# Kernel optimization log

Hardware: AMD Instinct MI355X
Metric: run time of the kernel (lower is better)

Reference implementation:

```python
import jax, jax.numpy as jnp
import numpy as np

B, K, E, D = 256, 2, 16, 512  # batch, top_k, num_experts, input_dim==output_dim
EPS = 1e-5  # nn.LayerNorm default eps
SCALE = 0.02  # param init scale


def setup_inputs() -> dict:
    key = jax.random.key(0)
    ks = jax.random.split(key, 9)
    return {
        "x": jax.random.normal(ks[0], (B, D), dtype=jnp.float32),
        "weight_probs": jax.random.uniform(ks[1], (B, K), dtype=jnp.float32),
        "bias_probs": jax.random.uniform(ks[2], (B, K), dtype=jnp.float32),
        "input_weight_bank": jax.random.normal(ks[3], (E, D, D), dtype=jnp.float32) * SCALE,
        "output_weight_bank": jax.random.normal(ks[4], (E, D, D), dtype=jnp.float32) * SCALE,
        "diagonal_weight_bank": jax.random.normal(ks[5], (E, D, D), dtype=jnp.float32) * SCALE,
        "bias_bank": jax.random.normal(ks[6], (E, D, D), dtype=jnp.float32) * SCALE,
        "weight_indices": jax.random.randint(ks[7], (B, K), 0, E),
        "bias_indices": jax.random.randint(ks[8], (B, K), 0, E),
    }


def reference(x, weight_probs, bias_probs, input_weight_bank, output_weight_bank,
              diagonal_weight_bank, bias_bank, weight_indices, bias_indices):
    # gather per-example expert parameter slabs: [B, K, D, D]
    iv = jnp.einsum('bi,bkij->bkj', x, input_weight_bank[weight_indices])     # [B,K,D]
    ov = jnp.einsum('bi,bkij->bkj', x, output_weight_bank[weight_indices])    # [B,K,D]
    dv = jnp.einsum('bi,bkij->bkj', x, diagonal_weight_bank[weight_indices])  # [B,K,D]

    # outer-product generated weight matrix + dynamic diagonal (in==out, no padding)
    outer = iv[..., :, None] * ov[..., None, :]                               # [B,K,D,D]
    r = jnp.arange(D)
    W = outer.at[..., r, r].add(dv)                                           # add diag embed

    # probability-weighted combine over top-k (weight_probs reshaped (-1,K,1,1) in torch)
    Wmix = jnp.einsum('bk,bkio->bio', weight_probs, W)                        # [B,D,D]

    # LayerNorm over output_dim, elementwise_affine=False
    mu = jnp.mean(Wmix, axis=-1, keepdims=True)
    var = jnp.var(Wmix, axis=-1, keepdims=True)
    Wn = (Wmix - mu) * jax.lax.rsqrt(var + EPS)

    # generated biases: gather + einsum + weighted combine ((-1,K,1) reshape)
    bv = jnp.einsum('bi,bkio->bko', x, bias_bank[bias_indices])               # [B,K,D]
    bmix = jnp.einsum('bk,bko->bo', bias_probs, bv)                           # [B,D]
    return (Wn, bmix)
```

## Files before the change

kernel.cpp:

```cpp
#include <hip/hip_runtime.h>
#include <math.h>

#define BB 256
#define KK 2
#define EE 16
#define DD 512
#define BK (BB*KK)
#define NP 4

#define WCH 18432
#define BCH 18560
#define WS_F_BASE 20480
#define SLAB (BK*DD)

__global__ void build_lists(const int* __restrict__ widx,
                            const int* __restrict__ bidx,
                            int* __restrict__ ws) {
    __shared__ int scw[16], scb[16];
    int* wlist = ws + 1024;
    int* blist = ws + 10240;
    const int t = threadIdx.x;
    if (t < 16) { scw[t] = 0; scb[t] = 0; }
    __syncthreads();
    int e = widx[t];
    int p = atomicAdd(&scw[e], 1);
    wlist[e * BK + p] = t;
    int eb = bidx[t];
    int pb = atomicAdd(&scb[eb], 1);
    blist[eb * BK + pb] = t;
    __syncthreads();
    if (t == 0) {
        int nc = 0;
        for (int e2 = 0; e2 < 16; ++e2) {
            int n = scw[e2];
            for (int r = 0; r < n; r += 16)
                ws[WCH + 1 + nc++] = e2 | (r << 8) | (min(16, n - r) << 20);
        }
        ws[WCH] = nc;
    }
    if (t == 64) {
        int nc = 0;
        for (int e2 = 0; e2 < 16; ++e2) {
            int n = scb[e2];
            for (int r = 0; r < n; r += 16)
                ws[BCH + 1 + nc++] = e2 | (r << 8) | (min(16, n - r) << 20);
        }
        ws[BCH] = nc;
    }
}

__launch_bounds__(256)
__global__ void expert_vm(const float* __restrict__ x,
                          const float* __restrict__ w_in,
                          const float* __restrict__ w_out,
                          const float* __restrict__ w_diag,
                          const float* __restrict__ w_bias,
                          const int* __restrict__ ws_i,
                          float* __restrict__ ws_f) {
    const int zp = blockIdx.z;
    const int z = zp >> 2, ip = zp & 3;
    const int* ch = ws_i + ((z < 3) ? WCH : BCH);
    const int slot = blockIdx.y;
    if (slot >= ch[0]) return;
    const int desc = ch[1 + slot];
    const int e = desc & 0xff, r0 = (desc >> 8) & 0xfff, rows = desc >> 20;
    const int* list = ws_i + ((z < 3) ? 1024 : 10240) + e * BK + r0;
    const int i0 = ip * 128;
    const float* W = (z == 0 ? w_in : z == 1 ? w_out : z == 2 ? w_diag : w_bias)
                     + (size_t)e * DD * DD + (size_t)i0 * DD;
    float* out = ws_f + WS_F_BASE + (size_t)zp * SLAB;

    __shared__ int plist[16];
    __shared__ float4 xs[128][4];
    const int t = threadIdx.x;
    if (t < 16) plist[t] = (t < rows) ? list[t] : -1;
    __syncthreads();
    #pragma unroll
    for (int k = 0; k < 2; ++k) {
        int idx = t + k * 256;
        int i = idx >> 2, q = idx & 3;
        int p0 = plist[q * 4 + 0], p1 = plist[q * 4 + 1];
        int p2 = plist[q * 4 + 2], p3 = plist[q * 4 + 3];
        float4 v;
        v.x = (p0 >= 0) ? x[(p0 >> 1) * DD + i0 + i] : 0.f;
        v.y = (p1 >= 0) ? x[(p1 >> 1) * DD + i0 + i] : 0.f;
        v.z = (p2 >= 0) ? x[(p2 >> 1) * DD + i0 + i] : 0.f;
        v.w = (p3 >= 0) ? x[(p3 >> 1) * DD + i0 + i] : 0.f;
        xs[i][q] = v;
    }
    __syncthreads();

    const int col = blockIdx.x * 128 + (t & 127);
    const int h = t >> 7;
    const float* Wc = W + col;
    float a0 = 0, a1 = 0, a2 = 0, a3 = 0, b0 = 0, b1 = 0, b2 = 0, b3 = 0;
    #pragma unroll 16
    for (int i = 0; i < 128; ++i) {
        float w = Wc[(size_t)i * DD];
        float4 xa = xs[i][2 * h];
        float4 xb = xs[i][2 * h + 1];
        a0 += xa.x * w; a1 += xa.y * w; a2 += xa.z * w; a3 += xa.w * w;
        b0 += xb.x * w; b1 += xb.y * w; b2 += xb.z * w; b3 += xb.w * w;
    }
    float accs[8] = {a0, a1, a2, a3, b0, b1, b2, b3};
    #pragma unroll
    for (int r = 0; r < 8; ++r) {
        int p = plist[h * 8 + r];
        if (p >= 0) out[(size_t)p * DD + col] = accs[r];
    }
}

__launch_bounds__(256)
__global__ void gen_write(const float* __restrict__ ws_f,
                          const float* __restrict__ wp,
                          float* __restrict__ outp) {
    const int b = blockIdx.y;
    const int chunk = blockIdx.x;
    const float* base = ws_f + WS_F_BASE;

    __shared__ float4 ov1v[128], ov2v[128];
    __shared__ float S[5], red[20];
    __shared__ float sa1[64], sa2[64], sdd[64], smu[64], srs[64];
    const int t = threadIdx.x;
    const float* ov1 = (const float*)ov1v;
    const float* ov2 = (const float*)ov2v;

    {
        const int tt = t & 127;
        const int row = b * 2 + (t >> 7);
        float sx = 0.f, sy = 0.f, sz = 0.f, sw = 0.f;
        #pragma unroll
        for (int pp = 0; pp < NP; ++pp) {
            const float4* q4 = (const float4*)(base + (size_t)(4 + pp) * SLAB
                                               + (size_t)row * DD);
            float4 v = q4[tt];
            sx += v.x; sy += v.y; sz += v.z; sw += v.w;
        }
        float4 s = make_float4(sx, sy, sz, sw);
        if (t < 128) ov1v[tt] = s; else ov2v[tt] = s;
    }
    __syncthreads();

    float v0a = ov1[t], v0b = ov1[t + 256], v1a = ov2[t], v1b = ov2[t + 256];
    float s[5];
    s[0] = v0a + v0b;
    s[1] = v1a + v1b;
    s[2] = v0a * v0a + v0b * v0b;
    s[3] = v0a * v1a + v0b * v1b;
    s[4] = v1a * v1a + v1b * v1b;
    #pragma unroll
    for (int off = 32; off; off >>= 1) {
        #pragma unroll
        for (int q = 0; q < 5; ++q) s[q] += __shfl_down(s[q], off);
    }
    const int lane = t & 63, wv = t >> 6;
    if (lane == 0) {
        #pragma unroll
        for (int q = 0; q < 5; ++q) red[wv * 5 + q] = s[q];
    }
    __syncthreads();
    if (t == 0) {
        #pragma unroll
        for (int q = 0; q < 5; ++q) S[q] = red[q] + red[5 + q] + red[10 + q] + red[15 + q];
    }
    __syncthreads();

    if (t < 64) {
        const float S1 = S[0], S2 = S[1], S11 = S[2], S12 = S[3], S22 = S[4];
        int i = chunk * 64 + t;
        float wp0 = wp[b * 2], wp1 = wp[b * 2 + 1];
        float iv1 = 0.f, iv2 = 0.f, dv1 = 0.f, dv2 = 0.f;
        #pragma unroll
        for (int pp = 0; pp < NP; ++pp) {
            const float* s0 = base + (size_t)(0 + pp) * SLAB;
            const float* s2 = base + (size_t)(8 + pp) * SLAB;
            iv1 += s0[(size_t)(b * 2 + 0) * DD + i];
            iv2 += s0[(size_t)(b * 2 + 1) * DD + i];
            dv1 += s2[(size_t)(b * 2 + 0) * DD + i];
            dv2 += s2[(size_t)(b * 2 + 1) * DD + i];
        }
        float a1 = wp0 * iv1;
        float a2 = wp1 * iv2;
        float dd = wp0 * dv1 + wp1 * dv2;
        float mu = (a1 * S1 + a2 * S2 + dd) * (1.0f / DD);
        float e2 = (a1 * a1 * S11 + 2.0f * a1 * a2 * S12 + a2 * a2 * S22
                    + 2.0f * (a1 * ov1[i] + a2 * ov2[i]) * dd + dd * dd) * (1.0f / DD);
        float var = e2 - mu * mu;
        sa1[t] = a1; sa2[t] = a2; sdd[t] = dd; smu[t] = mu;
        srs[t] = rsqrtf(var + 1e-5f);
    }
    __syncthreads();

    const int ci = t & 127, rh = t >> 7;
    const float4 o1 = ov1v[ci], o2 = ov2v[ci];
    const int jj = ci * 4;
    float* obase = outp + ((size_t)b * DD + chunk * 64) * DD;
    #pragma unroll 2
    for (int rr = 0; rr < 32; ++rr) {
        int r = rr * 2 + rh;
        int irow = chunk * 64 + r;
        float a1 = sa1[r], a2 = sa2[r], dd = sdd[r], mu = smu[r], rs = srs[r];
        float4 w;
        w.x = a1 * o1.x + a2 * o2.x + ((irow == jj)     ? dd : 0.f);
        w.y = a1 * o1.y + a2 * o2.y + ((irow == jj + 1) ? dd : 0.f);
        w.z = a1 * o1.z + a2 * o2.z + ((irow == jj + 2) ? dd : 0.f);
        w.w = a1 * o1.w + a2 * o2.w + ((irow == jj + 3) ? dd : 0.f);
        w.x = (w.x - mu) * rs; w.y = (w.y - mu) * rs;
        w.z = (w.z - mu) * rs; w.w = (w.w - mu) * rs;
        ((float4*)(obase + (size_t)r * DD))[ci] = w;
    }
}

__global__ void bias_mix(const float* __restrict__ ws_f,
                         const float* __restrict__ bp,
                         float* __restrict__ outp) {
    const float* base = ws_f + WS_F_BASE;
    int b = blockIdx.x;
    int t = threadIdx.x;
    float p0 = bp[b * 2], p1 = bp[b * 2 + 1];
    float s0a = 0.f, s0b = 0.f, s1a = 0.f, s1b = 0.f;
    #pragma unroll
    for (int pp = 0; pp < NP; ++pp) {
        const float* bv = base + (size_t)(12 + pp) * SLAB;
        s0a += bv[(size_t)(b * 2 + 0) * DD + t];
        s0b += bv[(size_t)(b * 2 + 0) * DD + t + 256];
        s1a += bv[(size_t)(b * 2 + 1) * DD + t];
        s1b += bv[(size_t)(b * 2 + 1) * DD + t + 256];
    }
    outp[(size_t)b * DD + t]       = p0 * s0a + p1 * s1a;
    outp[(size_t)b * DD + t + 256] = p0 * s0b + p1 * s1b;
}

extern "C" void kernel_launch(void* const* d_in, const int* in_sizes, int n_in,
                              void* d_out, int out_size, void* d_ws, size_t ws_size,
                              hipStream_t stream) {
    const float* x      = (const float*)d_in[0];
    const float* wprobs = (const float*)d_in[1];
    const float* bprobs = (const float*)d_in[2];
    const float* w_in   = (const float*)d_in[3];
    const float* w_out  = (const float*)d_in[4];
    const float* w_diag = (const float*)d_in[5];
    const float* w_bias = (const float*)d_in[6];
    const int*   widx   = (const int*)d_in[7];
    const int*   bidx   = (const int*)d_in[8];
    float* out = (float*)d_out;
    int*   wsI = (int*)d_ws;
    float* wsF = (float*)d_ws;

    build_lists<<<1, BK, 0, stream>>>(widx, bidx, wsI);

    expert_vm<<<dim3(4, 48, 16), 256, 0, stream>>>(x, w_in, w_out, w_diag, w_bias,
                                                   wsI, wsF);

    gen_write<<<dim3(8, BB), 256, 0, stream>>>(wsF, wprobs, out);

    bias_mix<<<BB, 256, 0, stream>>>(wsF, bprobs, out + (size_t)BB * DD * DD);
}
```

Baseline: 396.5 us.

## Widen expert_vm per-thread work, prefold LayerNorm scale, fuse bias_mix into gen_write

expert_vm now has each thread cover one column across all 16 list rows, so each weight element is loaded once per block instead of twice and the grid x-dimension is halved. gen_write precomputes per-row coefficients with the rsqrt folded in, so the inner loop becomes FMAs plus a diagonal add. The separate bias_mix kernel is removed and its work runs in the chunk-0 blocks of gen_write, saving one launch. The costs are higher register pressure from 16 accumulators and a small tail imbalance on the chunk-0 blocks.

After: 393.4 us. About the same (-0.8%).

```diff
diff --git a/kernel.cpp b/kernel.cpp
--- a/kernel.cpp
+++ b/kernel.cpp
@@ -90,37 +90,44 @@
     }
     __syncthreads();
 
-    const int col = blockIdx.x * 128 + (t & 127);
-    const int h = t >> 7;
+    const int col = blockIdx.x * 256 + t;
     const float* Wc = W + col;
-    float a0 = 0, a1 = 0, a2 = 0, a3 = 0, b0 = 0, b1 = 0, b2 = 0, b3 = 0;
-    #pragma unroll 16
+    float acc[16];
+    #pragma unroll
+    for (int r = 0; r < 16; ++r) acc[r] = 0.f;
+
+    #pragma unroll 8
     for (int i = 0; i < 128; ++i) {
         float w = Wc[(size_t)i * DD];
-        float4 xa = xs[i][2 * h];
-        float4 xb = xs[i][2 * h + 1];
-        a0 += xa.x * w; a1 += xa.y * w; a2 += xa.z * w; a3 += xa.w * w;
-        b0 += xb.x * w; b1 += xb.y * w; b2 += xb.z * w; b3 += xb.w * w;
-    }
-    float accs[8] = {a0, a1, a2, a3, b0, b1, b2, b3};
-    #pragma unroll
-    for (int r = 0; r < 8; ++r) {
-        int p = plist[h * 8 + r];
-        if (p >= 0) out[(size_t)p * DD + col] = accs[r];
+        float4 xa = xs[i][0];
+        float4 xb = xs[i][1];
+        float4 xc = xs[i][2];
+        float4 xd = xs[i][3];
+        acc[0]  += xa.x * w; acc[1]  += xa.y * w; acc[2]  += xa.z * w; acc[3]  += xa.w * w;
+        acc[4]  += xb.x * w; acc[5]  += xb.y * w; acc[6]  += xb.z * w; acc[7]  += xb.w * w;
+        acc[8]  += xc.x * w; acc[9]  += xc.y * w; acc[10] += xc.z * w; acc[11] += xc.w * w;
+        acc[12] += xd.x * w; acc[13] += xd.y * w; acc[14] += xd.z * w; acc[15] += xd.w * w;
+    }
+    #pragma unroll
+    for (int r = 0; r < 16; ++r) {
+        int p = plist[r];
+        if (p >= 0) out[(size_t)p * DD + col] = acc[r];
     }
 }
 
 __launch_bounds__(256)
 __global__ void gen_write(const float* __restrict__ ws_f,
                           const float* __restrict__ wp,
-                          float* __restrict__ outp) {
+                          const float* __restrict__ bp,
+                          float* __restrict__ outp,
+                          float* __restrict__ outb) {
     const int b = blockIdx.y;
     const int chunk = blockIdx.x;
     const float* base = ws_f + WS_F_BASE;
 
     __shared__ float4 ov1v[128], ov2v[128];
     __shared__ float S[5], red[20];
-    __shared__ float sa1[64], sa2[64], sdd[64], smu[64], srs[64];
+    __shared__ float saf1[64], saf2[64], scm[64], scc[64];
     const int t = threadIdx.x;
     const float* ov1 = (const float*)ov1v;
     const float* ov2 = (const float*)ov2v;
@@ -186,8 +193,11 @@
         float e2 = (a1 * a1 * S11 + 2.0f * a1 * a2 * S12 + a2 * a2 * S22
                     + 2.0f * (a1 * ov1[i] + a2 * ov2[i]) * dd + dd * dd) * (1.0f / DD);
         float var = e2 - mu * mu;
-        sa1[t] = a1; sa2[t] = a2; sdd[t] = dd; smu[t] = mu;
-        srs[t] = rsqrtf(var + 1e-5f);
+        float rs = rsqrtf(var + 1e-5f);
+        saf1[t] = a1 * rs;
+        saf2[t] = a2 * rs;
+        scm[t]  = -mu * rs;
+        scc[t]  = dd * rs;
     }
     __syncthreads();
 
@@ -199,36 +209,34 @@
     for (int rr = 0; rr < 32; ++rr) {
         int r = rr * 2 + rh;
         int irow = chunk * 64 + r;
-        float a1 = sa1[r], a2 = sa2[r], dd = sdd[r], mu = smu[r], rs = srs[r];
+        float af1 = saf1[r], af2 = saf2[r], cm = scm[r], cc = scc[r];
         float4 w;
-        w.x = a1 * o1.x + a2 * o2.x + ((irow == jj)     ? dd : 0.f);
-        w.y = a1 * o1.y + a2 * o2.y + ((irow == jj + 1) ? dd : 0.f);
-        w.z = a1 * o1.z + a2 * o2.z + ((irow == jj + 2) ? dd : 0.f);
-        w.w = a1 * o1.w + a2 * o2.w + ((irow == jj + 3) ? dd : 0.f);
-        w.x = (w.x - mu) * rs; w.y = (w.y - mu) * rs;
-        w.z = (w.z - mu) * rs; w.w = (w.w - mu) * rs;
+        w.x = fmaf(af1, o1.x, fmaf(af2, o2.x, cm));
+        w.y = fmaf(af1, o1.y, fmaf(af2, o2.y, cm));
+        w.z = fmaf(af1, o1.z, fmaf(af2, o2.z, cm));
+        w.w = fmaf(af1, o1.w, fmaf(af2, o2.w, cm));
+        int d = irow - jj;
+        w.x += (d == 0) ? cc : 0.f;
+        w.y += (d == 1) ? cc : 0.f;
+        w.z += (d == 2) ? cc : 0.f;
+        w.w += (d == 3) ? cc : 0.f;
         ((float4*)(obase + (size_t)r * DD))[ci] = w;
     }
-}
-
-__global__ void bias_mix(const float* __restrict__ ws_f,
-                         const float* __restrict__ bp,
-                         float* __restrict__ outp) {
-    const float* base = ws_f + WS_F_BASE;
-    int b = blockIdx.x;
-    int t = threadIdx.x;
-    float p0 = bp[b * 2], p1 = bp[b * 2 + 1];
-    float s0a = 0.f, s0b = 0.f, s1a = 0.f, s1b = 0.f;
-    #pragma unroll
-    for (int pp = 0; pp < NP; ++pp) {
-        const float* bv = base + (size_t)(12 + pp) * SLAB;
-        s0a += bv[(size_t)(b * 2 + 0) * DD + t];
-        s0b += bv[(size_t)(b * 2 + 0) * DD + t + 256];
-        s1a += bv[(size_t)(b * 2 + 1) * DD + t];
-        s1b += bv[(size_t)(b * 2 + 1) * DD + t + 256];
-    }
-    outp[(size_t)b * DD + t]       = p0 * s0a + p1 * s1a;
-    outp[(size_t)b * DD + t + 256] = p0 * s0b + p1 * s1b;
+
+    if (chunk == 0) {
+        float p0 = bp[b * 2], p1 = bp[b * 2 + 1];
+        float s0a = 0.f, s0b = 0.f, s1a = 0.f, s1b = 0.f;
+        #pragma unroll
+        for (int pp = 0; pp < NP; ++pp) {
+            const float* bv = base + (size_t)(12 + pp) * SLAB;
+            s0a += bv[(size_t)(b * 2 + 0) * DD + t];
+            s0b += bv[(size_t)(b * 2 + 0) * DD + t + 256];
+            s1a += bv[(size_t)(b * 2 + 1) * DD + t];
+            s1b += bv[(size_t)(b * 2 + 1) * DD + t + 256];
+        }
+        outb[(size_t)b * DD + t]       = p0 * s0a + p1 * s1a;
+        outb[(size_t)b * DD + t + 256] = p0 * s0b + p1 * s1b;
+    }
 }
 
 extern "C" void kernel_launch(void* const* d_in, const int* in_sizes, int n_in,
@@ -249,10 +257,9 @@
 
     build_lists<<<1, BK, 0, stream>>>(widx, bidx, wsI);
 
-    expert_vm<<<dim3(4, 48, 16), 256, 0, stream>>>(x, w_in, w_out, w_diag, w_bias,
+    expert_vm<<<dim3(2, 48, 16), 256, 0, stream>>>(x, w_in, w_out, w_diag, w_bias,
                                                    wsI, wsF);
 
-    gen_write<<<dim3(8, BB), 256, 0, stream>>>(wsF, wprobs, out);
-
-    bias_mix<<<BB, 256, 0, stream>>>(wsF, bprobs, out + (size_t)BB * DD * DD);
-}
+    gen_write<<<dim3(8, BB), 256, 0, stream>>>(wsF, wprobs, bprobs, out,
+                                               out + (size_t)BB * DD * DD);
+}
```
